# Optimization experiments

Measured on AMD Instinct MI355X. Metric: run time of the kernel, lower is better.

Reference implementation:

```python
import jax, jax.numpy as jnp
import numpy as np

EPS = 1e-05

def exp_map_at_origin(v, c):
    sqrt_c = jnp.sqrt(c)
    v_norm = jnp.maximum(jnp.linalg.norm(v, axis=-1, keepdims=True), EPS)
    return (1.0 / sqrt_c) * jnp.tanh(sqrt_c * v_norm) * (v / v_norm)

def log_map_at_origin(y, c):
    sqrt_c = jnp.sqrt(c)
    y_norm = jnp.maximum(jnp.linalg.norm(y, axis=-1, keepdims=True), EPS)
    y_norm_clamped = jnp.minimum(y_norm, 1.0 / sqrt_c - EPS)
    return (1.0 / sqrt_c) * jnp.arctanh(sqrt_c * y_norm_clamped) * (y / y_norm)

def poincare_distance(x, y, c):
    # x, y: [B, H, S, d]; returns [B, H, S, S]
    sqrt_c = jnp.sqrt(c)
    xns = jnp.sum(x * x, axis=-1, keepdims=True)          # [B,H,S,1]
    yns = jnp.sum(y * y, axis=-1, keepdims=True)          # [B,H,S,1]
    xy = jnp.einsum('bhsd,bhtd->bhst', x, y)
    xnsb = xns                                            # broadcast over t
    ynsb = jnp.swapaxes(yns, -2, -1)                      # [B,H,1,S]
    diff_norm_sq = xnsb - 2.0 * xy + ynsb
    denom = jnp.maximum((1.0 - c * xnsb) * (1.0 - c * ynsb), EPS)
    arg = jnp.maximum(1.0 + 2.0 * c * diff_norm_sq / denom, 1.0 + EPS)
    return (1.0 / sqrt_c) * jnp.arccosh(arg)

def setup_inputs() -> dict:
    key = jax.random.key(0)
    ks = jax.random.split(key, 5)
    B, S, D = 2, 1024, 1024
    x = jax.random.normal(ks[0], (B, S, D), dtype=jnp.float32)
    scale = 0.02
    W_q = scale * jax.random.normal(ks[1], (D, D), dtype=jnp.float32)
    W_k = scale * jax.random.normal(ks[2], (D, D), dtype=jnp.float32)
    W_v = scale * jax.random.normal(ks[3], (D, D), dtype=jnp.float32)
    W_o = scale * jax.random.normal(ks[4], (D, D), dtype=jnp.float32)
    return {
        'x': x, 'W_q': W_q, 'W_k': W_k, 'W_v': W_v, 'W_o': W_o,
        'log_c': jnp.zeros((), jnp.float32),
        'beta': jnp.zeros((), jnp.float32),
        'attention_bias': jnp.zeros((), jnp.float32),
    }

def reference(x, W_q, W_k, W_v, W_o, log_c, beta, attention_bias):
    B, S, D = x.shape
    H = 16
    dh = D // H
    c = jax.nn.softplus(log_c)
    beta_pos = jax.nn.softplus(beta)

    def split_heads(t):  # [B,S,D] -> [B,H,S,dh]
        return jnp.transpose(t.reshape(B, S, H, dh), (0, 2, 1, 3))

    q_t = split_heads(x @ W_q.T)
    k_t = split_heads(x @ W_k.T)
    v_t = split_heads(x @ W_v.T)

    q_h = exp_map_at_origin(q_t, c)
    k_h = exp_map_at_origin(k_t, c)
    v_h = exp_map_at_origin(v_t, c)

    dist = poincare_distance(q_h, k_h, c)                 # [B,H,S,S]
    scores = -beta_pos * dist - attention_bias
    weights = jax.nn.softmax(scores, axis=-1)

    v_tan = log_map_at_origin(v_h, c)
    out_tan = jnp.einsum('bhst,bhtd->bhsd', weights, v_tan)
    out_hyp = exp_map_at_origin(out_tan, c)
    out_heads_tan = log_map_at_origin(out_hyp, c)

    concat = jnp.transpose(out_heads_tan, (0, 2, 1, 3)).reshape(B, S, D)
    return concat @ W_o.T
```

## Files before the change

### kernel.cpp

```cpp
#include <hip/hip_runtime.h>
#include <math.h>


#define EPS_ 1e-5f

constexpr int Ss = 1024, Dd = 1024, Hh = 16, DHh = 64;

typedef __attribute__((ext_vector_type(8))) short bf16x8;
typedef __attribute__((ext_vector_type(4))) short s16x4;
typedef __attribute__((ext_vector_type(4))) float f32x4;

__device__ __forceinline__ float softplusf_(float x) {
    return (x > 20.f) ? x : log1pf(expf(x));
}
__device__ __forceinline__ float waveSum64(float v) {
#pragma unroll
    for (int m = 32; m >= 1; m >>= 1) v += __shfl_xor(v, m, 64);
    return v;
}
__device__ __forceinline__ short f2bf(float f) {
    union { float f; unsigned u; } v; v.f = f;
    unsigned r = v.u + 0x7FFFu + ((v.u >> 16) & 1u);
    return (short)(r >> 16);
}
__device__ __forceinline__ float bf2f(unsigned short h) {
    union { unsigned u; float f; } v; v.u = ((unsigned)h) << 16;
    return v.f;
}
__device__ __forceinline__ unsigned pks(short a, short b) {
    return (unsigned)(unsigned short)a | ((unsigned)(unsigned short)b << 16);
}

#if __has_builtin(__builtin_amdgcn_cvt_pk_bf16_f32)
typedef __attribute__((ext_vector_type(2))) __bf16 bfp2;
__device__ __forceinline__ unsigned cvtpk(float a, float b) {
    union { bfp2 v; unsigned u; } x;
    x.v = __builtin_amdgcn_cvt_pk_bf16_f32(a, b);
    return x.u;
}
#else
__device__ __forceinline__ unsigned cvtpk(float a, float b) { return pks(f2bf(a), f2bf(b)); }
#endif

#if __has_builtin(__builtin_amdgcn_sqrtf)
#define FSQRT __builtin_amdgcn_sqrtf
#else
#define FSQRT sqrtf
#endif
#if __has_builtin(__builtin_amdgcn_logf)
#define FLOG2 __builtin_amdgcn_logf
#else
#define FLOG2 __log2f
#endif
#if __has_builtin(__builtin_amdgcn_exp2f)
#define FEXP2 __builtin_amdgcn_exp2f
#else
#define FEXP2 exp2f
#endif

__global__ __launch_bounds__(256) void split_all(
    const float* __restrict__ x,  const float* __restrict__ Wq,
    const float* __restrict__ Wk, const float* __restrict__ Wv,
    const float* __restrict__ Wo,
    short* __restrict__ xh,  short* __restrict__ wqh,
    short* __restrict__ wkh, short* __restrict__ wvh, short* __restrict__ woh)
{
    int g = blockIdx.x * 256 + threadIdx.x;
    const float* src; short* dst; int base;
    if (g < 524288)       { src = x;  dst = xh;  base = g; }
    else if (g < 786432)  { src = Wq; dst = wqh; base = g - 524288; }
    else if (g < 1048576) { src = Wk; dst = wkh; base = g - 786432; }
    else if (g < 1310720) { src = Wv; dst = wvh; base = g - 1048576; }
    else                  { src = Wo; dst = woh; base = g - 1310720; }
    float4 v = *(const float4*)(src + (size_t)base * 4);
    uint2 hp; hp.x = cvtpk(v.x, v.y); hp.y = cvtpk(v.z, v.w);
    *(uint2*)(dst + (size_t)base * 4) = hp;
}

__global__ __launch_bounds__(256, 3) void gemm_qkv(
    const short* __restrict__ Ap,
    const short* __restrict__ Wq, const short* __restrict__ Wk, const short* __restrict__ Wv,
    short* __restrict__ qh, short* __restrict__ kh, short* __restrict__ vtT,
    float* __restrict__ qnsT, float2* __restrict__ knpk,
    const float* __restrict__ p_logc)
{
    const int z = blockIdx.z;
    const short* Bp = (z == 0) ? Wq : (z == 1 ? Wk : Wv);
    const int K = 1024;

    __shared__ short As[128 * 72];
    __shared__ short Bs[64 * 72];

    const int tid = threadIdx.x;
    const int wv = tid >> 6, lane = tid & 63, quad = lane >> 4, l15 = lane & 15;
    const int bm = blockIdx.y * 128, bn = blockIdx.x * 64;
    const int arow = tid >> 1, acol = (tid & 1) * 32;
    const int brow = tid >> 2, bcol = (tid & 3) * 16;

    const short* gA = Ap + (size_t)(bm + arow) * K + acol;
    const short* gB = Bp + (size_t)(bn + brow) * K + bcol;

    f32x4 acc[2][4];
#pragma unroll
    for (int mt = 0; mt < 2; mt++)
#pragma unroll
        for (int j = 0; j < 4; j++) acc[mt][j] = (f32x4){0.f, 0.f, 0.f, 0.f};

    bf16x8 a0 = *(const bf16x8*)gA;
    bf16x8 a1 = *(const bf16x8*)(gA + 8);
    bf16x8 a2 = *(const bf16x8*)(gA + 16);
    bf16x8 a3 = *(const bf16x8*)(gA + 24);
    bf16x8 b0 = *(const bf16x8*)gB;
    bf16x8 b1 = *(const bf16x8*)(gB + 8);

    for (int k0 = 0; k0 < K; k0 += 64) {
        __syncthreads();
        *(bf16x8*)&As[arow * 72 + acol]      = a0;
        *(bf16x8*)&As[arow * 72 + acol + 8]  = a1;
        *(bf16x8*)&As[arow * 72 + acol + 16] = a2;
        *(bf16x8*)&As[arow * 72 + acol + 24] = a3;
        *(bf16x8*)&Bs[brow * 72 + bcol]      = b0;
        *(bf16x8*)&Bs[brow * 72 + bcol + 8]  = b1;
        __syncthreads();
        if (k0 + 64 < K) {
            a0 = *(const bf16x8*)(gA + k0 + 64);
            a1 = *(const bf16x8*)(gA + k0 + 64 + 8);
            a2 = *(const bf16x8*)(gA + k0 + 64 + 16);
            a3 = *(const bf16x8*)(gA + k0 + 64 + 24);
            b0 = *(const bf16x8*)(gB + k0 + 64);
            b1 = *(const bf16x8*)(gB + k0 + 64 + 8);
        }
#pragma unroll
        for (int w = 0; w < 2; w++) {
            bf16x8 fa0 = *(const bf16x8*)&As[(wv * 32 + l15) * 72 + w * 32 + quad * 8];
            bf16x8 fa1 = *(const bf16x8*)&As[(wv * 32 + 16 + l15) * 72 + w * 32 + quad * 8];
#pragma unroll
            for (int nt = 0; nt < 4; nt++) {
                bf16x8 fb = *(const bf16x8*)&Bs[(nt * 16 + l15) * 72 + w * 32 + quad * 8];
                acc[0][nt] = __builtin_amdgcn_mfma_f32_16x16x32_bf16(fa0, fb, acc[0][nt], 0, 0, 0);
                acc[1][nt] = __builtin_amdgcn_mfma_f32_16x16x32_bf16(fa1, fb, acc[1][nt], 0, 0, 0);
            }
        }
    }

    const float c = softplusf_(p_logc[0]);
    const float sc = sqrtf(c);
    const float twoC = 2.f * c;
    const int h0 = blockIdx.x;

    if (z < 2) {
        short* yout = (z == 0) ? qh : kh;
#pragma unroll
        for (int mt = 0; mt < 2; mt++) {
            const int mbase = bm + wv * 32 + mt * 16;
            float fr[4];
#pragma unroll
            for (int r = 0; r < 4; r++) {
                float s2 = 0.f;
#pragma unroll
                for (int nt = 0; nt < 4; nt++) s2 += acc[mt][nt][r] * acc[mt][nt][r];
#pragma unroll
                for (int mk = 1; mk < 16; mk <<= 1) s2 += __shfl_xor(s2, mk, 64);
                float n = fmaxf(sqrtf(s2), EPS_);
                float fac = tanhf(sc * n) / (sc * n);
                fr[r] = fac;
                if (l15 == 0) {
                    int m = mbase + quad * 4 + r;
                    int bI = m >> 10, s = m & 1023;
                    float yns = s2 * fac * fac;
                    if (z == 0) {
                        qnsT[(size_t)(bI * Hh + h0) * Ss + s] = yns;
                    } else {
                        knpk[(size_t)(bI * Hh + h0) * Ss + s]
                            = make_float2(yns, twoC / (1.f - c * yns));
                    }
                }
            }
#pragma unroll
            for (int nt = 0; nt < 4; nt++)
#pragma unroll
                for (int r = 0; r < 4; r++) {
                    int m = mbase + quad * 4 + r;
                    yout[(size_t)m * Dd + bn + nt * 16 + l15] = f2bf(acc[mt][nt][r] * fr[r]);
                }
        }
    } else {
#pragma unroll
        for (int mt = 0; mt < 2; mt++) {
            const int mbase = bm + wv * 32 + mt * 16;
            float tr[4];
#pragma unroll
            for (int r = 0; r < 4; r++) {
                float s2 = 0.f;
#pragma unroll
                for (int nt = 0; nt < 4; nt++) s2 += acc[mt][nt][r] * acc[mt][nt][r];
#pragma unroll
                for (int mk = 1; mk < 16; mk <<= 1) s2 += __shfl_xor(s2, mk, 64);
                float n = fmaxf(sqrtf(s2), EPS_);
                float fac = tanhf(sc * n) / (sc * n);
                float yn = n * fac;
                float ycl = fminf(yn, 1.f / sc - EPS_);
                float f2 = atanhf(sc * ycl) / (sc * fmaxf(yn, EPS_));
                tr[r] = fac * f2;
            }
            const int m0 = mbase + quad * 4;
            const int bI = m0 >> 10, s0 = m0 & 1023;
#pragma unroll
            for (int nt = 0; nt < 4; nt++) {
                int d = nt * 16 + l15;
                uint2 pk;
                pk.x = cvtpk(acc[mt][nt][0] * tr[0], acc[mt][nt][1] * tr[1]);
                pk.y = cvtpk(acc[mt][nt][2] * tr[2], acc[mt][nt][3] * tr[3]);
                *(uint2*)&vtT[((size_t)(bI * Hh + h0) * DHh + d) * Ss + s0] = pk;
            }
        }
    }
}

__global__ __launch_bounds__(256) void attn_mfma(
    const short* __restrict__ qh, const short* __restrict__ kh, const short* __restrict__ vtT,
    const float* __restrict__ qnsT, const float2* __restrict__ knpk,
    unsigned short* __restrict__ Opart, float* __restrict__ lpart,
    const float* __restrict__ p_logc, const float* __restrict__ p_beta)
{
    const float c = softplusf_(p_logc[0]);
    const float sc = sqrtf(c);
    const float bp = softplusf_(p_beta[0]);
    const float nkc = -bp / sc;
    const float cap = 2.f * c * 1e5f;
    const float onePlus = 1.f + EPS_;

    const int h = blockIdx.y, b = blockIdx.z;
    const int kr = blockIdx.x & 3, qt = blockIdx.x >> 2;
    const int tid = threadIdx.x;
    const int wv = tid >> 6, lane = tid & 63;
    const int quad = lane >> 4, l15 = lane & 15;
    const int bh = b * Hh + h;
    const int q = qt * 64 + wv * 16 + l15;

    __shared__ short Ks[2][64][72];
    __shared__ short Vt[2][64][72];

    const short* qb = qh + (size_t)(b * Ss + q) * Dd + h * DHh + quad * 8;
    bf16x8 qf0 = *(const bf16x8*)qb;
    bf16x8 qf1 = *(const bf16x8*)(qb + 32);

    const float qn = qnsT[(size_t)bh * Ss + q];
    const float irq = 1.f / (1.f - c * qn);

    f32x4 O4[4];
#pragma unroll
    for (int nt = 0; nt < 4; nt++) O4[nt] = (f32x4){0.f, 0.f, 0.f, 0.f};
    float lac = 0.f;

    const int tbase = kr * 256;
    const int sr = tid >> 2, sseg = (tid & 3) * 16;
    const int vhi = sseg & 32;
    const int vup = (sseg & 16) ? 4 : 0;
    const short* kgp = kh + (size_t)(b * Ss + tbase + sr) * Dd + h * DHh + sseg;
    const short* vgp = vtT + ((size_t)bh * DHh + sr) * Ss + tbase + sseg;
    const float2* nb = knpk + (size_t)bh * Ss;

    bf16x8 kA0 = *(const bf16x8*)kgp;
    bf16x8 kA1 = *(const bf16x8*)(kgp + 8);
    bf16x8 vA0 = *(const bf16x8*)vgp;
    bf16x8 vA1 = *(const bf16x8*)(vgp + 8);
    {
        *(bf16x8*)&Ks[0][sr][sseg]     = kA0;
        *(bf16x8*)&Ks[0][sr][sseg + 8] = kA1;
        short* vrow = &Vt[0][sr][0];
        *(s16x4*)(vrow + vhi + vup)      = __builtin_shufflevector(vA0, vA0, 0, 1, 2, 3);
        *(s16x4*)(vrow + vhi + 8 + vup)  = __builtin_shufflevector(vA0, vA0, 4, 5, 6, 7);
        *(s16x4*)(vrow + vhi + 16 + vup) = __builtin_shufflevector(vA1, vA1, 0, 1, 2, 3);
        *(s16x4*)(vrow + vhi + 24 + vup) = __builtin_shufflevector(vA1, vA1, 4, 5, 6, 7);
    }
    __syncthreads();

    for (int ch = 0; ch < 4; ch++) {
        const int cur = ch & 1, nxt = cur ^ 1;
        const int t0 = tbase + ch * 64;

        if (ch < 3) {
            kA0 = *(const bf16x8*)(kgp + (size_t)((ch + 1) * 64) * Dd);
            kA1 = *(const bf16x8*)(kgp + (size_t)((ch + 1) * 64) * Dd + 8);
            vA0 = *(const bf16x8*)(vgp + (ch + 1) * 64);
            vA1 = *(const bf16x8*)(vgp + (ch + 1) * 64 + 8);
        }

        f32x4 n0[4], n1[4];
#pragma unroll
        for (int nt = 0; nt < 4; nt++) {
            const float2* np = nb + t0 + nt * 16 + quad * 4;
            n0[nt] = *(const f32x4*)np;
            n1[nt] = *(const f32x4*)(np + 2);
        }

        f32x4 acc[4];
#pragma unroll
        for (int nt = 0; nt < 4; nt++) {
            bf16x8 k0 = *(const bf16x8*)&Ks[cur][nt * 16 + l15][quad * 8];
            bf16x8 k1 = *(const bf16x8*)&Ks[cur][nt * 16 + l15][32 + quad * 8];
            f32x4 a = (f32x4){0.f, 0.f, 0.f, 0.f};
            a = __builtin_amdgcn_mfma_f32_16x16x32_bf16(k0, qf0, a, 0, 0, 0);
            a = __builtin_amdgcn_mfma_f32_16x16x32_bf16(k1, qf1, a, 0, 0, 0);
            acc[nt] = a;
        }

        float sv[4][4];
#pragma unroll
        for (int nt = 0; nt < 4; nt++) {
#pragma unroll
            for (int r = 0; r < 4; r++) {
                float kn   = (r < 2) ? n0[nt][(r & 1) * 2]     : n1[nt][(r & 1) * 2];
                float ik2c = (r < 2) ? n0[nt][(r & 1) * 2 + 1] : n1[nt][(r & 1) * 2 + 1];
                float dns = (qn + kn) - 2.f * acc[nt][r];
                float co  = fminf(irq * ik2c, cap);
                float arg = fmaxf(fmaf(co, dns, 1.f), onePlus);
                float u   = arg + FSQRT(fmaf(arg, arg, -1.f));
                float p   = FEXP2(nkc * FLOG2(u));
                sv[nt][r] = p;
                lac += p;
            }
        }

        union { unsigned u[4]; bf16x8 v; } p0, p1;
        p0.u[0] = cvtpk(sv[0][0], sv[0][1]); p0.u[1] = cvtpk(sv[0][2], sv[0][3]);
        p0.u[2] = cvtpk(sv[1][0], sv[1][1]); p0.u[3] = cvtpk(sv[1][2], sv[1][3]);
        p1.u[0] = cvtpk(sv[2][0], sv[2][1]); p1.u[1] = cvtpk(sv[2][2], sv[2][3]);
        p1.u[2] = cvtpk(sv[3][0], sv[3][1]); p1.u[3] = cvtpk(sv[3][2], sv[3][3]);

#pragma unroll
        for (int nt = 0; nt < 4; nt++) {
            bf16x8 v0 = *(const bf16x8*)&Vt[cur][nt * 16 + l15][quad * 8];
            bf16x8 v1 = *(const bf16x8*)&Vt[cur][nt * 16 + l15][32 + quad * 8];
            O4[nt] = __builtin_amdgcn_mfma_f32_16x16x32_bf16(v0, p0.v, O4[nt], 0, 0, 0);
            O4[nt] = __builtin_amdgcn_mfma_f32_16x16x32_bf16(v1, p1.v, O4[nt], 0, 0, 0);
        }

        if (ch < 3) {
            *(bf16x8*)&Ks[nxt][sr][sseg]     = kA0;
            *(bf16x8*)&Ks[nxt][sr][sseg + 8] = kA1;
            short* vrow = &Vt[nxt][sr][0];
            *(s16x4*)(vrow + vhi + vup)      = __builtin_shufflevector(vA0, vA0, 0, 1, 2, 3);
            *(s16x4*)(vrow + vhi + 8 + vup)  = __builtin_shufflevector(vA0, vA0, 4, 5, 6, 7);
            *(s16x4*)(vrow + vhi + 16 + vup) = __builtin_shufflevector(vA1, vA1, 0, 1, 2, 3);
            *(s16x4*)(vrow + vhi + 24 + vup) = __builtin_shufflevector(vA1, vA1, 4, 5, 6, 7);
            __syncthreads();
        }
    }

    lac += __shfl_xor(lac, 16, 64);
    lac += __shfl_xor(lac, 32, 64);
    unsigned short* ob = Opart + (((size_t)bh * 4 + kr) * Ss + q) * DHh;
#pragma unroll
    for (int nt = 0; nt < 4; nt++) {
        uint2 pk;
        pk.x = cvtpk(O4[nt][0], O4[nt][1]);
        pk.y = cvtpk(O4[nt][2], O4[nt][3]);
        *(uint2*)(ob + nt * 16 + quad * 4) = pk;
    }
    if (lane < 16)
        lpart[((size_t)bh * 4 + kr) * Ss + qt * 64 + wv * 16 + lane] = lac;
}

__global__ __launch_bounds__(256) void attn_combine(
    const unsigned short* __restrict__ Opart, const float* __restrict__ lpart,
    short* __restrict__ ccb, const float* __restrict__ p_logc)
{
    const float c = softplusf_(p_logc[0]);
    const float sc = sqrtf(c);
    const int wv = threadIdx.x >> 6, d = threadIdx.x & 63;
    const int task = blockIdx.x * 4 + wv;
    const int bh = task >> 10, s = task & 1023;

    float O = 0.f, l = 0.f;
#pragma unroll
    for (int k = 0; k < 4; k++) {
        O += bf2f(Opart[(((size_t)bh * 4 + k) * Ss + s) * DHh + d]);
        l += lpart[((size_t)bh * 4 + k) * Ss + s];
    }
    float ot = O / l;

    float t2 = waveSum64(ot * ot);
    float n = fmaxf(sqrtf(t2), EPS_);
    float fac = tanhf(sc * n) / (sc * n);
    float y2 = t2 * fac * fac;
    float yn = fmaxf(sqrtf(y2), EPS_);
    float ycl = fminf(yn, 1.f / sc - EPS_);
    float fac2 = atanhf(sc * ycl) / (sc * yn);
    float tot = fac * fac2;

    int b = bh >> 4, hh = bh & 15;
    ccb[(size_t)(b * Ss + s) * Dd + hh * DHh + d] = f2bf(ot * tot);
}

__global__ __launch_bounds__(256, 6) void gemm_out(
    const short* __restrict__ Ap, const short* __restrict__ Bp,
    float* __restrict__ Cp)
{
    const int K = 1024, N = 1024;
    __shared__ short As[64 * 72];
    __shared__ short Bs[64 * 72];
    const int tid = threadIdx.x;
    const int wv = tid >> 6, lane = tid & 63, quad = lane >> 4, l15 = lane & 15;
    const int bm = blockIdx.y * 64, bn = blockIdx.x * 64;
    const int sr = tid >> 2, sq = (tid & 3) * 16;

    const short* gA = Ap + (size_t)(bm + sr) * K + sq;
    const short* gB = Bp + (size_t)(bn + sr) * K + sq;

    f32x4 acc[4];
#pragma unroll
    for (int j = 0; j < 4; j++) acc[j] = (f32x4){0.f, 0.f, 0.f, 0.f};

    bf16x8 a0 = *(const bf16x8*)gA;
    bf16x8 a1 = *(const bf16x8*)(gA + 8);
    bf16x8 b0 = *(const bf16x8*)gB;
    bf16x8 b1 = *(const bf16x8*)(gB + 8);

    for (int k0 = 0; k0 < K; k0 += 64) {
        __syncthreads();
        *(bf16x8*)&As[sr * 72 + sq]     = a0;
        *(bf16x8*)&As[sr * 72 + sq + 8] = a1;
        *(bf16x8*)&Bs[sr * 72 + sq]     = b0;
        *(bf16x8*)&Bs[sr * 72 + sq + 8] = b1;
        __syncthreads();
        if (k0 + 64 < K) {
            a0 = *(const bf16x8*)(gA + k0 + 64);
            a1 = *(const bf16x8*)(gA + k0 + 64 + 8);
            b0 = *(const bf16x8*)(gB + k0 + 64);
            b1 = *(const bf16x8*)(gB + k0 + 64 + 8);
        }
#pragma unroll
        for (int w = 0; w < 2; w++) {
            bf16x8 fa = *(const bf16x8*)&As[(wv * 16 + l15) * 72 + w * 32 + quad * 8];
#pragma unroll
            for (int nt = 0; nt < 4; nt++) {
                bf16x8 fb = *(const bf16x8*)&Bs[(nt * 16 + l15) * 72 + w * 32 + quad * 8];
                acc[nt] = __builtin_amdgcn_mfma_f32_16x16x32_bf16(fa, fb, acc[nt], 0, 0, 0);
            }
        }
    }
#pragma unroll
    for (int nt = 0; nt < 4; nt++)
#pragma unroll
        for (int r = 0; r < 4; r++)
            Cp[(size_t)(bm + wv * 16 + quad * 4 + r) * N + bn + nt * 16 + l15] = acc[nt][r];
}

extern "C" void kernel_launch(void* const* d_in, const int* in_sizes, int n_in,
                              void* d_out, int out_size, void* d_ws, size_t ws_size,
                              hipStream_t stream)
{
    const float* x    = (const float*)d_in[0];
    const float* Wq   = (const float*)d_in[1];
    const float* Wk   = (const float*)d_in[2];
    const float* Wv   = (const float*)d_in[3];
    const float* Wo   = (const float*)d_in[4];
    const float* logc = (const float*)d_in[5];
    const float* beta = (const float*)d_in[6];
    float* out = (float*)d_out;

    const size_t M2 = 2097152, M1 = 1048576;
    short* ws    = (short*)d_ws;
    short* xh    = ws;
    short* wqh   = xh + M2;
    short* wkh   = wqh + M1;
    short* wvh   = wkh + M1;
    short* woh   = wvh + M1;
    short* qh    = woh + M1;
    short* kh    = qh + M2;
    short* vtT   = kh + M2;
    float* qnsT  = (float*)(vtT + M2);
    float2* knpk = (float2*)(qnsT + 32768);
    float* lpart = (float*)(knpk + 32768);
    unsigned short* Opart = (unsigned short*)(lpart + 131072);
    short* ccb   = xh;

    split_all<<<dim3(6144), 256, 0, stream>>>(x, Wq, Wk, Wv, Wo, xh, wqh, wkh, wvh, woh);
    gemm_qkv<<<dim3(16, 16, 3), 256, 0, stream>>>(xh, wqh, wkh, wvh,
        qh, kh, vtT, qnsT, knpk, logc);
    attn_mfma<<<dim3(64, 16, 2), 256, 0, stream>>>(qh, kh, vtT, qnsT, knpk,
        Opart, lpart, logc, beta);
    attn_combine<<<dim3(8192), 256, 0, stream>>>(Opart, lpart, ccb, logc);
    gemm_out<<<dim3(16, 32), 256, 0, stream>>>(ccb, woh, out);
}
```

Baseline: 175.4 us.

## Load GEMM tiles straight into LDS with XOR swizzle instead of register staging

The QKV and output-projection GEMMs now copy bf16 tiles from global memory directly into LDS with the global_load_lds builtin, replacing the register staging and the padded stride-72 layout. An XOR swizzle on 16-byte chunks lets the MFMA fragment reads avoid bank conflicts without padding. The old register prefetch of the next tile is removed, so loads are no longer overlapped with compute. The only thing hiding load latency is other resident blocks, and the direct-to-LDS path needs a wait at the barrier before the tile is read.

```diff
diff --git a/kernel.cpp b/kernel.cpp
--- a/kernel.cpp
+++ b/kernel.cpp
@@ -58,6 +58,12 @@
 #define FEXP2 exp2f
 #endif
 
+__device__ __forceinline__ void gload_lds16(const short* gp, short* lp) {
+    __builtin_amdgcn_global_load_lds(
+        (__attribute__((address_space(1))) void*)(void*)(const_cast<short*>(gp)),
+        (__attribute__((address_space(3))) void*)(void*)(lp), 16, 0, 0);
+}
+
 __global__ __launch_bounds__(256) void split_all(
     const float* __restrict__ x,  const float* __restrict__ Wq,
     const float* __restrict__ Wk, const float* __restrict__ Wv,
@@ -88,55 +94,42 @@
     const short* Bp = (z == 0) ? Wq : (z == 1 ? Wk : Wv);
     const int K = 1024;
 
-    __shared__ short As[128 * 72];
-    __shared__ short Bs[64 * 72];
+    __shared__ short As[128 * 64];
+    __shared__ short Bs[64 * 64];
 
     const int tid = threadIdx.x;
     const int wv = tid >> 6, lane = tid & 63, quad = lane >> 4, l15 = lane & 15;
     const int bm = blockIdx.y * 128, bn = blockIdx.x * 64;
-    const int arow = tid >> 1, acol = (tid & 1) * 32;
-    const int brow = tid >> 2, bcol = (tid & 3) * 16;
-
-    const short* gA = Ap + (size_t)(bm + arow) * K + acol;
-    const short* gB = Bp + (size_t)(bn + brow) * K + bcol;
+
+    const int lr8 = lane >> 3, lc8 = lane & 7;
+    const int swz8 = (lc8 ^ lr8) * 8;
+
+    const short* gAl = Ap + (size_t)(bm + lr8) * K + swz8;
+    const short* gBl = Bp + (size_t)(bn + lr8) * K + swz8;
 
     f32x4 acc[2][4];
 #pragma unroll
     for (int mt = 0; mt < 2; mt++)
 #pragma unroll
         for (int j = 0; j < 4; j++) acc[mt][j] = (f32x4){0.f, 0.f, 0.f, 0.f};
-
-    bf16x8 a0 = *(const bf16x8*)gA;
-    bf16x8 a1 = *(const bf16x8*)(gA + 8);
-    bf16x8 a2 = *(const bf16x8*)(gA + 16);
-    bf16x8 a3 = *(const bf16x8*)(gA + 24);
-    bf16x8 b0 = *(const bf16x8*)gB;
-    bf16x8 b1 = *(const bf16x8*)(gB + 8);
 
     for (int k0 = 0; k0 < K; k0 += 64) {
         __syncthreads();
-        *(bf16x8*)&As[arow * 72 + acol]      = a0;
-        *(bf16x8*)&As[arow * 72 + acol + 8]  = a1;
-        *(bf16x8*)&As[arow * 72 + acol + 16] = a2;
-        *(bf16x8*)&As[arow * 72 + acol + 24] = a3;
-        *(bf16x8*)&Bs[brow * 72 + bcol]      = b0;
-        *(bf16x8*)&Bs[brow * 72 + bcol + 8]  = b1;
+#pragma unroll
+        for (int i = 0; i < 4; i++)
+            gload_lds16(gAl + (size_t)((wv * 4 + i) * 8) * K + k0, &As[(wv * 4 + i) * 512]);
+#pragma unroll
+        for (int j = 0; j < 2; j++)
+            gload_lds16(gBl + (size_t)((wv * 2 + j) * 8) * K + k0, &Bs[(wv * 2 + j) * 512]);
         __syncthreads();
-        if (k0 + 64 < K) {
-            a0 = *(const bf16x8*)(gA + k0 + 64);
-            a1 = *(const bf16x8*)(gA + k0 + 64 + 8);
-            a2 = *(const bf16x8*)(gA + k0 + 64 + 16);
-            a3 = *(const bf16x8*)(gA + k0 + 64 + 24);
-            b0 = *(const bf16x8*)(gB + k0 + 64);
-            b1 = *(const bf16x8*)(gB + k0 + 64 + 8);
-        }
 #pragma unroll
         for (int w = 0; w < 2; w++) {
-            bf16x8 fa0 = *(const bf16x8*)&As[(wv * 32 + l15) * 72 + w * 32 + quad * 8];
-            bf16x8 fa1 = *(const bf16x8*)&As[(wv * 32 + 16 + l15) * 72 + w * 32 + quad * 8];
+            const int xs = ((w * 4 + quad) ^ (l15 & 7)) * 8;
+            bf16x8 fa0 = *(const bf16x8*)&As[(wv * 32 + l15) * 64 + xs];
+            bf16x8 fa1 = *(const bf16x8*)&As[(wv * 32 + 16 + l15) * 64 + xs];
 #pragma unroll
             for (int nt = 0; nt < 4; nt++) {
-                bf16x8 fb = *(const bf16x8*)&Bs[(nt * 16 + l15) * 72 + w * 32 + quad * 8];
+                bf16x8 fb = *(const bf16x8*)&Bs[(nt * 16 + l15) * 64 + xs];
                 acc[0][nt] = __builtin_amdgcn_mfma_f32_16x16x32_bf16(fa0, fb, acc[0][nt], 0, 0, 0);
                 acc[1][nt] = __builtin_amdgcn_mfma_f32_16x16x32_bf16(fa1, fb, acc[1][nt], 0, 0, 0);
             }
@@ -399,44 +392,37 @@
     float* __restrict__ Cp)
 {
     const int K = 1024, N = 1024;
-    __shared__ short As[64 * 72];
-    __shared__ short Bs[64 * 72];
+    __shared__ short As[64 * 64];
+    __shared__ short Bs[64 * 64];
     const int tid = threadIdx.x;
     const int wv = tid >> 6, lane = tid & 63, quad = lane >> 4, l15 = lane & 15;
     const int bm = blockIdx.y * 64, bn = blockIdx.x * 64;
-    const int sr = tid >> 2, sq = (tid & 3) * 16;
-
-    const short* gA = Ap + (size_t)(bm + sr) * K + sq;
-    const short* gB = Bp + (size_t)(bn + sr) * K + sq;
+
+    const int lr8 = lane >> 3, lc8 = lane & 7;
+    const int swz8 = (lc8 ^ lr8) * 8;
+
+    const short* gAl = Ap + (size_t)(bm + lr8) * K + swz8;
+    const short* gBl = Bp + (size_t)(bn + lr8) * K + swz8;
 
     f32x4 acc[4];
 #pragma unroll
     for (int j = 0; j < 4; j++) acc[j] = (f32x4){0.f, 0.f, 0.f, 0.f};
-
-    bf16x8 a0 = *(const bf16x8*)gA;
-    bf16x8 a1 = *(const bf16x8*)(gA + 8);
-    bf16x8 b0 = *(const bf16x8*)gB;
-    bf16x8 b1 = *(const bf16x8*)(gB + 8);
 
     for (int k0 = 0; k0 < K; k0 += 64) {
         __syncthreads();
-        *(bf16x8*)&As[sr * 72 + sq]     = a0;
-        *(bf16x8*)&As[sr * 72 + sq + 8] = a1;
-        *(bf16x8*)&Bs[sr * 72 + sq]     = b0;
-        *(bf16x8*)&Bs[sr * 72 + sq + 8] = b1;
+#pragma unroll
+        for (int j = 0; j < 2; j++) {
+            gload_lds16(gAl + (size_t)((wv * 2 + j) * 8) * K + k0, &As[(wv * 2 + j) * 512]);
+            gload_lds16(gBl + (size_t)((wv * 2 + j) * 8) * K + k0, &Bs[(wv * 2 + j) * 512]);
+        }
         __syncthreads();
-        if (k0 + 64 < K) {
-            a0 = *(const bf16x8*)(gA + k0 + 64);
-            a1 = *(const bf16x8*)(gA + k0 + 64 + 8);
-            b0 = *(const bf16x8*)(gB + k0 + 64);
-            b1 = *(const bf16x8*)(gB + k0 + 64 + 8);
-        }
 #pragma unroll
         for (int w = 0; w < 2; w++) {
-            bf16x8 fa = *(const bf16x8*)&As[(wv * 16 + l15) * 72 + w * 32 + quad * 8];
+            const int xs = ((w * 4 + quad) ^ (l15 & 7)) * 8;
+            bf16x8 fa = *(const bf16x8*)&As[(wv * 16 + l15) * 64 + xs];
 #pragma unroll
             for (int nt = 0; nt < 4; nt++) {
-                bf16x8 fb = *(const bf16x8*)&Bs[(nt * 16 + l15) * 72 + w * 32 + quad * 8];
+                bf16x8 fb = *(const bf16x8*)&Bs[(nt * 16 + l15) * 64 + xs];
                 acc[nt] = __builtin_amdgcn_mfma_f32_16x16x32_bf16(fa, fb, acc[nt], 0, 0, 0);
             }
         }
```

After: 172.1 us. Within noise of the previous version (-1.9%).
